# Performance work log

Measured on AMD Instinct MI355X. Metric: run time of the kernel, lower is better.

## Reference

```python
import jax, jax.numpy as jnp
import numpy as np

B, D_IN = 16384, 1024
NUM_LAYERS, K, CB_DIM = 4, 1024, 512


def setup_inputs() -> dict:
    key = jax.random.key(0)
    ks = jax.random.split(key, 6)
    return {
        "dense_content_embedding": jax.random.normal(ks[0], (B, D_IN), jnp.float32),
        "enc_W": jax.random.normal(ks[1], (D_IN, CB_DIM), jnp.float32) / np.sqrt(D_IN),
        "enc_b": jnp.zeros((CB_DIM,), jnp.float32),
        "codebooks": jax.random.normal(ks[2], (NUM_LAYERS, K, CB_DIM), jnp.float32),
        "dec_W": jax.random.normal(ks[3], (NUM_LAYERS, CB_DIM), jnp.float32) / np.sqrt(NUM_LAYERS),
        "dec_b": jnp.zeros((CB_DIM,), jnp.float32),
    }


def reference(dense_content_embedding, enc_W, enc_b, codebooks, dec_W, dec_b):
    # encoder: Dense(codebook_dim)
    r0 = dense_content_embedding @ enc_W + enc_b  # [B, CB_DIM]

    def step(residual, cb):
        # squared L2 distance: ||r||^2 - 2 r.c + ||c||^2  -> [B, K]
        d = (jnp.sum(residual * residual, axis=-1, keepdims=True)
             - 2.0 * (residual @ cb.T)
             + jnp.sum(cb * cb, axis=-1))
        idx = jnp.argmin(d, axis=-1)            # [B]
        next_residual = residual - cb[idx]      # gather + residual update
        return next_residual, idx

    _, ids = jax.lax.scan(step, r0, codebooks)  # ids: [L, B]
    semantic_ids = ids.T                        # [B, L] (stack along axis=1)

    # decoder: Dense(codebook_dim) applied to the integer ids (as in source)
    recon = semantic_ids.astype(r0.dtype) @ dec_W + dec_b  # [B, CB_DIM]
    return recon, semantic_ids
```

## Files before the change

kernel.cpp:

```cpp
#include <hip/hip_runtime.h>
#include <float.h>
#include <limits.h>

#define BB 16384
#define DIN 1024
#define CB 512
#define KC 1024
#define NL 4

#define DELTA 0.25f

typedef __attribute__((ext_vector_type(8))) _Float16 half8;
typedef __attribute__((ext_vector_type(8))) short bf16x8;
typedef __attribute__((ext_vector_type(8))) unsigned short us8;
typedef __attribute__((ext_vector_type(4))) float f32x4;

__device__ __forceinline__ unsigned short f2h(float f) {
  _Float16 h = (_Float16)f;
  return *(unsigned short*)&h;
}

__device__ __forceinline__ unsigned short f2b(float f) {
  unsigned u = __float_as_uint(f);
  unsigned r = u + 0x7fffu + ((u >> 16) & 1u);
  return (unsigned short)(r >> 16);
}
__device__ __forceinline__ float b2f(unsigned short h) {
  return __uint_as_float(((unsigned)h) << 16);
}

__device__ __forceinline__ unsigned cvtpk_bf16(float a, float b) {
  unsigned r;
  asm("v_cvt_pk_bf16_f32 %0, %1, %2" : "=v"(r) : "v"(a), "v"(b));
  return r;
}

__device__ __forceinline__ size_t staged_off(int row, int k) {
  return ((size_t)(row >> 4) * 16 + (k >> 5)) * 512 +
         (((k >> 3) & 3) * 16 + (row & 15)) * 8 + (k & 7);
}

__device__ __forceinline__ size_t staged_off_w(int row, int k) {
  return ((size_t)(row >> 4) * 32 + (k >> 5)) * 512 +
         (((k >> 3) & 3) * 16 + (row & 15)) * 8 + (k & 7);
}


__global__ __launch_bounds__(256) void cbsplit_kernel(
    const float* __restrict__ cbs, unsigned short* __restrict__ Ch16) {
  int g = (blockIdx.x * 256 + threadIdx.x) * 4;
  int k = g & (CB - 1);
  int lr = g >> 9;
  int layer = lr >> 10, row = lr & (KC - 1);
  float4 v = *(const float4*)(cbs + g);
  size_t off = (size_t)layer * (KC / 16) * 8192 + staged_off(row, k);
  *(ushort4*)(Ch16 + off) = make_ushort4(f2h(v.x), f2h(v.y), f2h(v.z), f2h(v.w));
}

__global__ __launch_bounds__(256) void wsplit_kernel(
    const float* __restrict__ W, unsigned short* __restrict__ WTh,
    unsigned short* __restrict__ WTm) {
  int g = blockIdx.x * 256 + threadIdx.x;
  int n = g >> 8;
  int k0 = (g & 255) * 4;
  ushort4 h4, m4;
  unsigned short* hp = (unsigned short*)&h4;
  unsigned short* mp = (unsigned short*)&m4;
#pragma unroll
  for (int i = 0; i < 4; ++i) {
    float x = W[(size_t)(k0 + i) * CB + n];
    unsigned short h = f2b(x);
    hp[i] = h;
    mp[i] = f2b(x - b2f(h));
  }
  size_t off = staged_off_w(n, k0);
  *(ushort4*)(WTh + off) = h4;
  *(ushort4*)(WTm + off) = m4;
}

__global__ __launch_bounds__(256) void cnorm_kernel(
    const float* __restrict__ cbs, double* __restrict__ cnorm,
    float* __restrict__ cnormF) {
  int gw = (blockIdx.x * blockDim.x + threadIdx.x) >> 6;
  int lane = threadIdx.x & 63;
  if (gw >= NL * KC) return;
  const float* row = cbs + (size_t)gw * CB;
  double s = 0.0;
  for (int i = lane; i < CB; i += 64) {
    double v = (double)row[i];
    s += v * v;
  }
#pragma unroll
  for (int off = 32; off > 0; off >>= 1)
    s += __shfl_down(s, off, 64);
  if (lane == 0) { cnorm[gw] = s; cnormF[gw] = (float)s; }
}

__global__ __launch_bounds__(256, 2) void enc_gemm(
    const float* __restrict__ X, const unsigned short* __restrict__ WTh,
    const unsigned short* __restrict__ WTm, const float* __restrict__ bias,
    float* __restrict__ R, unsigned short* __restrict__ Rh16) {
  __shared__ __align__(16) char lds[65536];
  int tid = threadIdx.x;
  int wave = tid >> 6, lane = tid & 63;
  int wm = wave >> 1, wn = wave & 1;
  int q = lane >> 4, l15 = lane & 15;
  int bx = blockIdx.x;
  int rb = ((bx & 7) << 1) + ((bx >> 3) & 1) + ((bx >> 6) << 4);
  int cbk = (bx >> 4) & 3;
  int row0 = rb * 128, n0 = cbk * 128;

  int ar = tid >> 1;
  int aq = (tid & 1) * 16;
  const float* xsrc = X + (size_t)(row0 + ar) * DIN + aq;
  int awoff = (ar >> 4) * 1024 + (((aq >> 3) & 3) * 16 + (ar & 15)) * 16;

  f32x4 acc[4][4];
#pragma unroll
  for (int i = 0; i < 4; ++i)
#pragma unroll
    for (int j = 0; j < 4; ++j)
      acc[i][j] = (f32x4){0.f, 0.f, 0.f, 0.f};

  float xv[16];
  unsigned hp[8], mp[8];

#define LOADX(c)                                         \
  {                                                      \
    _Pragma("unroll") for (int j = 0; j < 4; ++j) {      \
      float4 v = *(const float4*)(xsrc + (c) * 32 + j * 4); \
      xv[4 * j + 0] = v.x; xv[4 * j + 1] = v.y;          \
      xv[4 * j + 2] = v.z; xv[4 * j + 3] = v.w;          \
    }                                                    \
  }
#define SPLITX()                                            \
  {                                                         \
    _Pragma("unroll") for (int j = 0; j < 8; ++j) {         \
      float x0 = xv[2 * j], x1 = xv[2 * j + 1];             \
      unsigned h = cvtpk_bf16(x0, x1);                      \
      float h0 = __uint_as_float(h << 16);                  \
      float h1 = __uint_as_float(h & 0xffff0000u);          \
      hp[j] = h;                                            \
      mp[j] = cvtpk_bf16(x0 - h0, x1 - h1);                 \
    }                                                       \
  }
#define WRITEA(bufbase)                                                     \
  {                                                                         \
    *(uint4*)(lds + (bufbase) + awoff) =                                    \
        make_uint4(hp[0], hp[1], hp[2], hp[3]);                             \
    *(uint4*)(lds + (bufbase) + awoff + 256) =                              \
        make_uint4(hp[4], hp[5], hp[6], hp[7]);                             \
    *(uint4*)(lds + (bufbase) + awoff + 8192) =                             \
        make_uint4(mp[0], mp[1], mp[2], mp[3]);                             \
    *(uint4*)(lds + (bufbase) + awoff + 8192 + 256) =                       \
        make_uint4(mp[4], mp[5], mp[6], mp[7]);                             \
  }
#define ISSUEB(ktile, bufbase)                                               \
  {                                                                          \
    _Pragma("unroll") for (int i = 0; i < 4; ++i) {                          \
      int c = wave * 4 + i;                                                  \
      const unsigned short* bsrc = (c < 8) ? WTh : WTm;                      \
      int rg = (n0 >> 4) + (c & 7);                                         \
      __builtin_amdgcn_global_load_lds(                                      \
          (const __attribute__((address_space(1))) void*)(                   \
              bsrc + ((size_t)rg * 32 + (ktile)) * 512 + lane * 8),          \
          (__attribute__((address_space(3))) void*)(                         \
              lds + (bufbase) + 16384 + c * 1024),                           \
          16, 0, 0);                                                         \
    }                                                                        \
  }

  LOADX(0); SPLITX();
  ISSUEB(0, 0);
  WRITEA(0);
  LOADX(1); SPLITX();
  __syncthreads();

  for (int kt = 0; kt < 32; ++kt) {
    int cur = kt & 1;
    int nb = (cur ^ 1) << 15;
    if (kt < 31) {
      ISSUEB(kt + 1, nb);
      WRITEA(nb);
    }
    if (kt < 30) LOADX(kt + 2);

    const char* cb0 = lds + (cur << 15);
    bf16x8 ah[4], am[4];
#pragma unroll
    for (int ti = 0; ti < 4; ++ti) {
      ah[ti] = *(const bf16x8*)(cb0 + (wm * 4 + ti) * 1024 + lane * 16);
      am[ti] = *(const bf16x8*)(cb0 + 8192 + (wm * 4 + ti) * 1024 + lane * 16);
    }
#pragma unroll
    for (int tj = 0; tj < 4; ++tj) {
      bf16x8 bh = *(const bf16x8*)(cb0 + 16384 + (wn * 4 + tj) * 1024 + lane * 16);
      bf16x8 bm = *(const bf16x8*)(cb0 + 24576 + (wn * 4 + tj) * 1024 + lane * 16);
#pragma unroll
      for (int ti = 0; ti < 4; ++ti)
        acc[ti][tj] = __builtin_amdgcn_mfma_f32_16x16x32_bf16(ah[ti], bh, acc[ti][tj], 0, 0, 0);
#pragma unroll
      for (int ti = 0; ti < 4; ++ti)
        acc[ti][tj] = __builtin_amdgcn_mfma_f32_16x16x32_bf16(am[ti], bh, acc[ti][tj], 0, 0, 0);
#pragma unroll
      for (int ti = 0; ti < 4; ++ti)
        acc[ti][tj] = __builtin_amdgcn_mfma_f32_16x16x32_bf16(ah[ti], bm, acc[ti][tj], 0, 0, 0);
    }
    if (kt < 30) SPLITX();
    __syncthreads();
  }

#pragma unroll
  for (int ti = 0; ti < 4; ++ti) {
#pragma unroll
    for (int tj = 0; tj < 4; ++tj) {
      int col = n0 + wn * 64 + tj * 16 + l15;
      float bv = bias[col];
#pragma unroll
      for (int r = 0; r < 4; ++r) {
        int row = row0 + wm * 64 + ti * 16 + q * 4 + r;
        float val = acc[ti][tj][r] + bv;
        R[(size_t)row * CB + col] = val;
        Rh16[staged_off(row, col)] = f2h(val);
      }
    }
  }
#undef LOADX
#undef SPLITX
#undef WRITEA
#undef ISSUEB
}

__global__ __launch_bounds__(256, 2) void vq_stage1(
    const unsigned short* __restrict__ Rh16,
    const unsigned short* __restrict__ Ch16,
    const float* __restrict__ cnormF, float4* __restrict__ cand) {
  __shared__ __align__(16) char lds[49152];
  int tid = threadIdx.x;
  int wave = tid >> 6, lane = tid & 63;
  int q = lane >> 4, l15 = lane & 15;
  int g = blockIdx.x;
  int rb = (g & 7) + ((g >> 6) << 3);
  int cbk = (g >> 3) & 7;
  int row0 = rb * 256, n0 = cbk * 128;

  f32x4 acc[4][8];
#pragma unroll
  for (int i = 0; i < 4; ++i)
#pragma unroll
    for (int j = 0; j < 8; ++j)
      acc[i][j] = (f32x4){0.f, 0.f, 0.f, 0.f};

  const unsigned short* gA =
      Rh16 + ((size_t)(row0 >> 4) + wave * 4) * 8192 + lane * 8;
  const unsigned short* gB =
      Ch16 + ((size_t)(n0 >> 4) + wave * 2) * 8192 + lane * 8;
  char* lA = lds + wave * 4 * 1024;
  char* lB = lds + 16384 + wave * 2 * 1024;

#define STAGE1_ISSUE(ktile, bufbase)                                         \
  {                                                                          \
    _Pragma("unroll") for (int s = 0; s < 4; ++s) {                          \
      __builtin_amdgcn_global_load_lds(                                      \
          (const __attribute__((address_space(1))) void*)(                   \
              gA + (size_t)s * 8192 + (ktile) * 512),                        \
          (__attribute__((address_space(3))) void*)(lA + (bufbase) + s * 1024), \
          16, 0, 0);                                                         \
    }                                                                        \
    _Pragma("unroll") for (int s = 0; s < 2; ++s) {                          \
      __builtin_amdgcn_global_load_lds(                                      \
          (const __attribute__((address_space(1))) void*)(                   \
              gB + (size_t)s * 8192 + (ktile) * 512),                        \
          (__attribute__((address_space(3))) void*)(lB + (bufbase) + s * 1024), \
          16, 0, 0);                                                         \
    }                                                                        \
  }

  STAGE1_ISSUE(0, 0);
  __syncthreads();

  for (int kt = 0; kt < 16; ++kt) {
    int cur = kt & 1;
    if (kt < 15) STAGE1_ISSUE(kt + 1, (cur ^ 1) * 24576);
    const char* ca = lds + cur * 24576;
    const char* cbp = ca + 16384;
    half8 af[4];
#pragma unroll
    for (int ri = 0; ri < 4; ++ri)
      af[ri] = *(const half8*)(ca + (wave * 4 + ri) * 1024 + lane * 16);
#pragma unroll
    for (int tj = 0; tj < 8; ++tj) {
      half8 b = *(const half8*)(cbp + tj * 1024 + lane * 16);
#pragma unroll
      for (int ri = 0; ri < 4; ++ri)
        acc[ri][tj] = __builtin_amdgcn_mfma_f32_16x16x32_f16(af[ri], b, acc[ri][tj], 0, 0, 0);
    }
    __syncthreads();
  }
#undef STAGE1_ISSUE

  float cn[8]; int coln[8];
#pragma unroll
  for (int tj = 0; tj < 8; ++tj) {
    coln[tj] = n0 + tj * 16 + l15;
    cn[tj] = cnormF[coln[tj]];
  }
#pragma unroll
  for (int ri = 0; ri < 4; ++ri) {
#pragma unroll
    for (int r = 0; r < 4; ++r) {
      unsigned long long k1 = ~0ull, k2 = ~0ull;
#pragma unroll
      for (int tj = 0; tj < 8; ++tj) {
        float v = cn[tj] - 2.0f * acc[ri][tj][r];
        unsigned u = __float_as_uint(v);
        u = (u & 0x80000000u) ? ~u : (u | 0x80000000u);
        unsigned long long key =
            ((unsigned long long)u << 32) | (unsigned)coln[tj];
        if (key < k1) { k2 = k1; k1 = key; }
        else if (key < k2) { k2 = key; }
      }
#pragma unroll
      for (int mask = 1; mask <= 8; mask <<= 1) {
        unsigned long long o1 = __shfl_xor(k1, mask, 64);
        unsigned long long o2 = __shfl_xor(k2, mask, 64);
        if (o1 < k1) { k2 = (k1 < o2) ? k1 : o2; k1 = o1; }
        else { k2 = (k2 < o1) ? k2 : o1; }
      }
      if (l15 == 0) {
        unsigned s1 = (unsigned)(k1 >> 32), s2 = (unsigned)(k2 >> 32);
        unsigned b1 = (s1 & 0x80000000u) ? (s1 ^ 0x80000000u) : ~s1;
        unsigned b2 = (s2 & 0x80000000u) ? (s2 ^ 0x80000000u) : ~s2;
        int row = row0 + wave * 64 + ri * 16 + q * 4 + r;
        cand[(size_t)row * 8 + cbk] = make_float4(
            __uint_as_float(b1), __int_as_float((int)(unsigned)k1),
            __uint_as_float(b2), __int_as_float((int)(unsigned)k2));
      }
    }
  }
}

__global__ __launch_bounds__(256) void vq_refine(
    const float* __restrict__ cb, const double* __restrict__ cnorm,
    const float4* __restrict__ cand, float* __restrict__ R,
    unsigned short* __restrict__ Rh16, float* __restrict__ idsF, int layer) {
  __shared__ int sIdx[32][16];
  __shared__ int sCnt[32];
  __shared__ int sBest[32];
  __shared__ int sPair[512];
  __shared__ int sNP;
  __shared__ double sD[32][16];

  int tid = threadIdx.x;
  int b = blockIdx.x;
  int v = ((b & 7) << 3) + ((b >> 3) & 7) + ((b >> 6) << 6);
  int row0 = v * 32;

  if (tid == 0) sNP = 0;
  __syncthreads();

  if (tid < 32) {
    int row = row0 + tid;
    float vv[16]; int ix[16];
#pragma unroll
    for (int c = 0; c < 8; ++c) {
      float4 e = cand[(size_t)row * 8 + c];
      vv[2 * c] = e.x;     ix[2 * c] = __float_as_int(e.y);
      vv[2 * c + 1] = e.z; ix[2 * c + 1] = __float_as_int(e.w);
    }
    float M = FLT_MAX; int I = INT_MAX;
#pragma unroll
    for (int p = 0; p < 16; ++p)
      if (vv[p] < M || (vv[p] == M && ix[p] < I)) { M = vv[p]; I = ix[p]; }
    int cnt = 0;
#pragma unroll
    for (int p = 0; p < 16; ++p)
      if (vv[p] < M + DELTA && cnt < 16) sIdx[tid][cnt++] = ix[p];
    sCnt[tid] = cnt;
    sBest[tid] = I;
    if (cnt >= 2) {
      int base = atomicAdd(&sNP, cnt);
      for (int c = 0; c < cnt; ++c) sPair[base + c] = (tid << 4) | c;
    }
  }
  __syncthreads();

  int np = sNP;
  int wave = tid >> 6, lane = tid & 63;
  for (int p = wave; p < np; p += 4) {
    int pr = sPair[p];
    int r = pr >> 4, c = pr & 15;
    int idx = sIdx[r][c];
    const float* rrow = R + (size_t)(row0 + r) * CB;
    const float* crow = cb + (size_t)idx * CB;
    double s = 0.0;
#pragma unroll
    for (int e = 0; e < CB; e += 64)
      s += (double)rrow[e + lane] * (double)crow[e + lane];
#pragma unroll
    for (int off = 32; off > 0; off >>= 1)
      s += __shfl_xor(s, off, 64);
    if (lane == 0) sD[r][c] = cnorm[idx] - 2.0 * s;
  }
  __syncthreads();

  if (tid < 32) {
    int cnt = sCnt[tid];
    if (cnt >= 2) {
      double bestD = 1e300; int bestI = INT_MAX;
      for (int c = 0; c < cnt; ++c) {
        double d = sD[tid][c]; int idx = sIdx[tid][c];
        if (d < bestD || (d == bestD && idx < bestI)) { bestD = d; bestI = idx; }
      }
      sBest[tid] = bestI;
    }
    idsF[(size_t)(row0 + tid) * NL + layer] = (float)sBest[tid];
  }
  __syncthreads();

  for (int it = tid; it < 32 * (CB / 4); it += 256) {
    int r = it >> 7, dq = (it & 127) * 4;
    int row = row0 + r;
    size_t o = (size_t)row * CB + dq;
    float4 rv = *(const float4*)(R + o);
    const float* crow = cb + (size_t)sBest[r] * CB + dq;
    float nv[4] = {rv.x - crow[0], rv.y - crow[1], rv.z - crow[2], rv.w - crow[3]};
    *(float4*)(R + o) = make_float4(nv[0], nv[1], nv[2], nv[3]);
    size_t so = staged_off(row, dq);
    *(ushort4*)(Rh16 + so) =
        make_ushort4(f2h(nv[0]), f2h(nv[1]), f2h(nv[2]), f2h(nv[3]));
  }
}

__global__ __launch_bounds__(256) void recon_kernel(
    const float* __restrict__ idsF, const float* __restrict__ decW,
    const float* __restrict__ decb, float* __restrict__ recon) {
  int g = blockIdx.x * 256 + threadIdx.x;
  int b = g >> 9, j = g & (CB - 1);
  float s = decb[j];
#pragma unroll
  for (int l = 0; l < NL; ++l)
    s += idsF[(size_t)b * NL + l] * decW[l * CB + j];
  recon[g] = s;
}

extern "C" void kernel_launch(void* const* d_in, const int* in_sizes, int n_in,
                              void* d_out, int out_size, void* d_ws, size_t ws_size,
                              hipStream_t stream) {
  const float* X    = (const float*)d_in[0];
  const float* encW = (const float*)d_in[1];
  const float* encb = (const float*)d_in[2];
  const float* cbs  = (const float*)d_in[3];
  const float* decW = (const float*)d_in[4];
  const float* decb = (const float*)d_in[5];

  float* out = (float*)d_out;
  float* recon = out;
  float* idsF = out + (size_t)BB * CB;

  char* ws = (char*)d_ws;
  float* R = (float*)ws;                     ws += (size_t)BB * CB * 4;
  unsigned short* Rh16 = (unsigned short*)ws; ws += (size_t)BB * CB * 2;
  unsigned short* Ch16 = (unsigned short*)ws; ws += (size_t)NL * KC * CB * 2;
  double* cnorm = (double*)ws;               ws += (size_t)NL * KC * 8;
  float* cnormF = (float*)ws;                ws += (size_t)NL * KC * 4;
  float4* cand = (float4*)ws;                ws += (size_t)BB * 8 * 16;
  unsigned short* WTh = (unsigned short*)ws; ws += (size_t)CB * DIN * 2;
  unsigned short* WTm = (unsigned short*)ws;

  cbsplit_kernel<<<(NL * KC * CB) / 1024, 256, 0, stream>>>(cbs, Ch16);
  cnorm_kernel<<<(NL * KC) / 4, 256, 0, stream>>>(cbs, cnorm, cnormF);
  wsplit_kernel<<<(CB * DIN / 4) / 256, 256, 0, stream>>>(encW, WTh, WTm);
  enc_gemm<<<(BB / 128) * (CB / 128), 256, 0, stream>>>(X, WTh, WTm, encb, R, Rh16);
  for (int l = 0; l < NL; ++l) {
    const float* cbl = cbs + (size_t)l * KC * CB;
    vq_stage1<<<(BB / 256) * 8, 256, 0, stream>>>(
        Rh16, Ch16 + (size_t)l * KC * CB, cnormF + (size_t)l * KC, cand);
    vq_refine<<<BB / 32, 256, 0, stream>>>(cbl, cnorm + (size_t)l * KC, cand,
                                           R, Rh16, idsF, l);
  }
  recon_kernel<<<(BB * CB) / 256, 256, 0, stream>>>(idsF, decW, decb, recon);
}
```

Baseline: 385.0 us.

## Load per-wave GEMM operands directly into registers instead of staging through LDS

In the encoder GEMM, the B (weight hi/lo) fragments each wave uses are now loaded from global memory straight into double-buffered registers instead of being copied into LDS with global_load_lds. In VQ stage 1, the A (residual) fragments get the same treatment. This shrinks LDS per block (64KB to 32KB and 48KB to 16KB) and removes the LDS reads for those operands, which could help occupancy. The cost is more VGPRs and global loads that may be less coalesced or less reused. Operands that other waves in the block share are no longer loaded once into LDS, so they may be fetched several times from global memory or L2.

```diff
diff --git a/kernel.cpp b/kernel.cpp
--- a/kernel.cpp
+++ b/kernel.cpp
@@ -100,7 +100,7 @@
     const float* __restrict__ X, const unsigned short* __restrict__ WTh,
     const unsigned short* __restrict__ WTm, const float* __restrict__ bias,
     float* __restrict__ R, unsigned short* __restrict__ Rh16) {
-  __shared__ __align__(16) char lds[65536];
+  __shared__ __align__(16) char lds[32768];
   int tid = threadIdx.x;
   int wave = tid >> 6, lane = tid & 63;
   int wm = wave >> 1, wn = wave & 1;
@@ -115,6 +115,11 @@
   const float* xsrc = X + (size_t)(row0 + ar) * DIN + aq;
   int awoff = (ar >> 4) * 1024 + (((aq >> 3) & 3) * 16 + (ar & 15)) * 16;
 
+  const char* bph = (const char*)WTh +
+                    ((size_t)((n0 >> 4) + wn * 4) * 32) * 1024 + lane * 16;
+  const char* bpm = (const char*)WTm +
+                    ((size_t)((n0 >> 4) + wn * 4) * 32) * 1024 + lane * 16;
+
   f32x4 acc[4][4];
 #pragma unroll
   for (int i = 0; i < 4; ++i)
@@ -124,6 +129,7 @@
 
   float xv[16];
   unsigned hp[8], mp[8];
+  uint4 BHa[4], BMa[4], BHb[4], BMb[4];
 
 #define LOADX(c)                                         \
   {                                                      \
@@ -155,59 +161,49 @@
     *(uint4*)(lds + (bufbase) + awoff + 8192 + 256) =                       \
         make_uint4(mp[4], mp[5], mp[6], mp[7]);                             \
   }
-#define ISSUEB(ktile, bufbase)                                               \
-  {                                                                          \
-    _Pragma("unroll") for (int i = 0; i < 4; ++i) {                          \
-      int c = wave * 4 + i;                                                  \
-      const unsigned short* bsrc = (c < 8) ? WTh : WTm;                      \
-      int rg = (n0 >> 4) + (c & 7);                                         \
-      __builtin_amdgcn_global_load_lds(                                      \
-          (const __attribute__((address_space(1))) void*)(                   \
-              bsrc + ((size_t)rg * 32 + (ktile)) * 512 + lane * 8),          \
-          (__attribute__((address_space(3))) void*)(                         \
-              lds + (bufbase) + 16384 + c * 1024),                           \
-          16, 0, 0);                                                         \
-    }                                                                        \
+#define BLOADTO(ktile, BH, BM)                                              \
+  {                                                                         \
+    _Pragma("unroll") for (int tj = 0; tj < 4; ++tj) {                      \
+      BH[tj] = *(const uint4*)(bph + (size_t)tj * 32768 + (size_t)(ktile) * 1024); \
+      BM[tj] = *(const uint4*)(bpm + (size_t)tj * 32768 + (size_t)(ktile) * 1024); \
+    }                                                                       \
+  }
+#define ESTEP(kt, CB_, NB_, BHc, BMc, BHn, BMn)                             \
+  {                                                                         \
+    if ((kt) < 31) {                                                        \
+      WRITEA(NB_);                                                          \
+      BLOADTO((kt) + 1, BHn, BMn);                                          \
+    }                                                                       \
+    if ((kt) < 30) LOADX((kt) + 2);                                         \
+    const char* cb0 = lds + (CB_);                                          \
+    bf16x8 ah[4], am[4];                                                    \
+    _Pragma("unroll") for (int ti = 0; ti < 4; ++ti) {                      \
+      ah[ti] = *(const bf16x8*)(cb0 + (wm * 4 + ti) * 1024 + lane * 16);    \
+      am[ti] = *(const bf16x8*)(cb0 + 8192 + (wm * 4 + ti) * 1024 + lane * 16); \
+    }                                                                       \
+    _Pragma("unroll") for (int tj = 0; tj < 4; ++tj) {                      \
+      bf16x8 bh = *(const bf16x8*)&BHc[tj];                                 \
+      bf16x8 bm = *(const bf16x8*)&BMc[tj];                                 \
+      _Pragma("unroll") for (int ti = 0; ti < 4; ++ti)                      \
+        acc[ti][tj] = __builtin_amdgcn_mfma_f32_16x16x32_bf16(ah[ti], bh, acc[ti][tj], 0, 0, 0); \
+      _Pragma("unroll") for (int ti = 0; ti < 4; ++ti)                      \
+        acc[ti][tj] = __builtin_amdgcn_mfma_f32_16x16x32_bf16(am[ti], bh, acc[ti][tj], 0, 0, 0); \
+      _Pragma("unroll") for (int ti = 0; ti < 4; ++ti)                      \
+        acc[ti][tj] = __builtin_amdgcn_mfma_f32_16x16x32_bf16(ah[ti], bm, acc[ti][tj], 0, 0, 0); \
+    }                                                                       \
+    if ((kt) < 30) SPLITX();                                                \
+    __syncthreads();                                                        \
   }
 
   LOADX(0); SPLITX();
-  ISSUEB(0, 0);
   WRITEA(0);
+  BLOADTO(0, BHa, BMa);
   LOADX(1); SPLITX();
   __syncthreads();
 
-  for (int kt = 0; kt < 32; ++kt) {
-    int cur = kt & 1;
-    int nb = (cur ^ 1) << 15;
-    if (kt < 31) {
-      ISSUEB(kt + 1, nb);
-      WRITEA(nb);
-    }
-    if (kt < 30) LOADX(kt + 2);
-
-    const char* cb0 = lds + (cur << 15);
-    bf16x8 ah[4], am[4];
-#pragma unroll
-    for (int ti = 0; ti < 4; ++ti) {
-      ah[ti] = *(const bf16x8*)(cb0 + (wm * 4 + ti) * 1024 + lane * 16);
-      am[ti] = *(const bf16x8*)(cb0 + 8192 + (wm * 4 + ti) * 1024 + lane * 16);
-    }
-#pragma unroll
-    for (int tj = 0; tj < 4; ++tj) {
-      bf16x8 bh = *(const bf16x8*)(cb0 + 16384 + (wn * 4 + tj) * 1024 + lane * 16);
-      bf16x8 bm = *(const bf16x8*)(cb0 + 24576 + (wn * 4 + tj) * 1024 + lane * 16);
-#pragma unroll
-      for (int ti = 0; ti < 4; ++ti)
-        acc[ti][tj] = __builtin_amdgcn_mfma_f32_16x16x32_bf16(ah[ti], bh, acc[ti][tj], 0, 0, 0);
-#pragma unroll
-      for (int ti = 0; ti < 4; ++ti)
-        acc[ti][tj] = __builtin_amdgcn_mfma_f32_16x16x32_bf16(am[ti], bh, acc[ti][tj], 0, 0, 0);
-#pragma unroll
-      for (int ti = 0; ti < 4; ++ti)
-        acc[ti][tj] = __builtin_amdgcn_mfma_f32_16x16x32_bf16(ah[ti], bm, acc[ti][tj], 0, 0, 0);
-    }
-    if (kt < 30) SPLITX();
-    __syncthreads();
+  for (int kt2 = 0; kt2 < 16; ++kt2) {
+    ESTEP(2 * kt2,     0,     16384, BHa, BMa, BHb, BMb);
+    ESTEP(2 * kt2 + 1, 16384, 0,     BHb, BMb, BHa, BMa);
   }
 
 #pragma unroll
@@ -228,14 +224,15 @@
 #undef LOADX
 #undef SPLITX
 #undef WRITEA
-#undef ISSUEB
+#undef BLOADTO
+#undef ESTEP
 }
 
 __global__ __launch_bounds__(256, 2) void vq_stage1(
     const unsigned short* __restrict__ Rh16,
     const unsigned short* __restrict__ Ch16,
     const float* __restrict__ cnormF, float4* __restrict__ cand) {
-  __shared__ __align__(16) char lds[49152];
+  __shared__ __align__(16) char lds[16384];
   int tid = threadIdx.x;
   int wave = tid >> 6, lane = tid & 63;
   int q = lane >> 4, l15 = lane & 15;
@@ -251,22 +248,14 @@
     for (int j = 0; j < 8; ++j)
       acc[i][j] = (f32x4){0.f, 0.f, 0.f, 0.f};
 
-  const unsigned short* gA =
-      Rh16 + ((size_t)(row0 >> 4) + wave * 4) * 8192 + lane * 8;
+  const char* aptr = (const char*)Rh16 +
+                     ((size_t)(row0 >> 4) + wave * 4) * 16 * 1024 + lane * 16;
   const unsigned short* gB =
       Ch16 + ((size_t)(n0 >> 4) + wave * 2) * 8192 + lane * 8;
-  char* lA = lds + wave * 4 * 1024;
-  char* lB = lds + 16384 + wave * 2 * 1024;
-
-#define STAGE1_ISSUE(ktile, bufbase)                                         \
+  char* lB = lds + wave * 2 * 1024;
+
+#define S1_ISSUEB(ktile, bufbase)                                            \
   {                                                                          \
-    _Pragma("unroll") for (int s = 0; s < 4; ++s) {                          \
-      __builtin_amdgcn_global_load_lds(                                      \
-          (const __attribute__((address_space(1))) void*)(                   \
-              gA + (size_t)s * 8192 + (ktile) * 512),                        \
-          (__attribute__((address_space(3))) void*)(lA + (bufbase) + s * 1024), \
-          16, 0, 0);                                                         \
-    }                                                                        \
     _Pragma("unroll") for (int s = 0; s < 2; ++s) {                          \
       __builtin_amdgcn_global_load_lds(                                      \
           (const __attribute__((address_space(1))) void*)(                   \
@@ -275,29 +264,40 @@
           16, 0, 0);                                                         \
     }                                                                        \
   }
-
-  STAGE1_ISSUE(0, 0);
-  __syncthreads();
-
-  for (int kt = 0; kt < 16; ++kt) {
-    int cur = kt & 1;
-    if (kt < 15) STAGE1_ISSUE(kt + 1, (cur ^ 1) * 24576);
-    const char* ca = lds + cur * 24576;
-    const char* cbp = ca + 16384;
-    half8 af[4];
-#pragma unroll
-    for (int ri = 0; ri < 4; ++ri)
-      af[ri] = *(const half8*)(ca + (wave * 4 + ri) * 1024 + lane * 16);
-#pragma unroll
-    for (int tj = 0; tj < 8; ++tj) {
-      half8 b = *(const half8*)(cbp + tj * 1024 + lane * 16);
-#pragma unroll
-      for (int ri = 0; ri < 4; ++ri)
-        acc[ri][tj] = __builtin_amdgcn_mfma_f32_16x16x32_f16(af[ri], b, acc[ri][tj], 0, 0, 0);
-    }
-    __syncthreads();
-  }
-#undef STAGE1_ISSUE
+#define ALOADTO(ktile, A)                                                    \
+  {                                                                          \
+    _Pragma("unroll") for (int ri = 0; ri < 4; ++ri)                         \
+      A[ri] = *(const uint4*)(aptr + (size_t)ri * 16384 + (size_t)(ktile) * 1024); \
+  }
+#define S1STEP(kt, CURB, NXTB, Ac, An)                                       \
+  {                                                                          \
+    if ((kt) < 15) {                                                         \
+      S1_ISSUEB((kt) + 1, NXTB);                                             \
+      ALOADTO((kt) + 1, An);                                                 \
+    }                                                                        \
+    const char* cbp = lds + (CURB);                                          \
+    _Pragma("unroll") for (int tj = 0; tj < 8; ++tj) {                       \
+      half8 b = *(const half8*)(cbp + tj * 1024 + lane * 16);                \
+      _Pragma("unroll") for (int ri = 0; ri < 4; ++ri)                       \
+        acc[ri][tj] = __builtin_amdgcn_mfma_f32_16x16x32_f16(                \
+            *(const half8*)&Ac[ri], b, acc[ri][tj], 0, 0, 0);                \
+    }                                                                        \
+    __syncthreads();                                                         \
+  }
+
+  uint4 Aa[4], Ab[4];
+
+  S1_ISSUEB(0, 0);
+  ALOADTO(0, Aa);
+  __syncthreads();
+
+  for (int kt2 = 0; kt2 < 8; ++kt2) {
+    S1STEP(2 * kt2,     0,    8192, Aa, Ab);
+    S1STEP(2 * kt2 + 1, 8192, 0,    Ab, Aa);
+  }
+#undef S1_ISSUEB
+#undef ALOADTO
+#undef S1STEP
 
   float cn[8]; int coln[8];
 #pragma unroll
```

Result: no change. 387.9 us (+0.7%).
